# Performance work log

Measured on AMD Instinct MI355X. Metric: run time of the kernel, lower is better.

Reference implementation:

```python
import jax, jax.numpy as jnp
import numpy as np

DIM = 1024
HEADS = 16
HD = DIM // HEADS          # 64
HID = 4 * DIM              # 4096
TPF = 1374                 # tokens_per_frame
LR = 0.1
NS_ITERS = 5
TTT_STEPS = 2
B, S = 2, 4
SN = S * TPF               # 5496


def _newton_schulz(G, iters=NS_ITERS):
    """Muon Newton-Schulz orthogonalization (quintic iteration)."""
    a, b, c = 3.4445, -4.7750, 2.0315
    X = G / (jnp.linalg.norm(G) + 1e-7)
    transposed = G.shape[0] > G.shape[1]
    if transposed:
        X = X.T
    for _ in range(iters):
        A = X @ X.T                      # [m,m], m = min(rows, cols)
        X = a * X + (b * A + c * (A @ A)) @ X
    return X.T if transposed else X


def _muon_update(p, g):
    return p - LR * _newton_schulz(g)


def setup_inputs() -> dict:
    key = jax.random.key(0)
    ks = jax.random.split(key, 8)
    inp = {
        "x": jax.random.normal(ks[0], (B, SN, DIM), jnp.float32),
        "qkv_w": jax.random.normal(ks[1], (DIM, 3 * DIM), jnp.float32) * (DIM ** -0.5),
        "qkv_b": jnp.zeros((3 * DIM,), jnp.float32),
        "qn_scale": jnp.ones((HD,), jnp.float32),
        "qn_bias": jnp.zeros((HD,), jnp.float32),
        "kn_scale": jnp.ones((HD,), jnp.float32),
        "kn_bias": jnp.zeros((HD,), jnp.float32),
        # theta: lecun-normal scale (std = 1/sqrt(fan_in))
        "ttt_gate": jax.random.normal(ks[2], (DIM, HID), jnp.float32) * (DIM ** -0.5),
        "ttt_val": jax.random.normal(ks[3], (DIM, HID), jnp.float32) * (DIM ** -0.5),
        "ttt_proj": jax.random.normal(ks[4], (HID, DIM), jnp.float32) * (HID ** -0.5),
        "proj_w": jax.random.normal(ks[5], (DIM, DIM), jnp.float32) * (DIM ** -0.5),
        "proj_b": jnp.zeros((DIM,), jnp.float32),
    }
    return inp


def reference(x, qkv_w, qkv_b, qn_scale, qn_bias, kn_scale, kn_bias,
              ttt_gate, ttt_val, ttt_proj, proj_w, proj_b):
    Bx, SNx, _ = x.shape
    qkv = x @ qkv_w + qkv_b                       # [B, SN, 3*DIM]
    q, k, v = jnp.split(qkv, 3, axis=-1)
    q = q.reshape(Bx, SNx, HEADS, HD)
    k = k.reshape(Bx, SNx, HEADS, HD)
    # per-head L2 normalize then affine NormLayer (x*scale + bias)
    q = q / (jnp.linalg.norm(q, axis=-1, keepdims=True) + 1e-6) * qn_scale + qn_bias
    k = k / (jnp.linalg.norm(k, axis=-1, keepdims=True) + 1e-6) * kn_scale + kn_bias
    q_ttt = q.reshape(-1, DIM)                    # [B*SN, DIM]
    k_ttt = k.reshape(-1, DIM)
    # no short_conv param at init -> v_mixed is identity, so v_target == v
    v_ttt = v.reshape(-1, DIM)

    theta = {"gate": ttt_gate, "val": ttt_val, "proj": ttt_proj}

    def loss_fn(p):
        h = jax.nn.swish(k_ttt @ p["gate"]) * (k_ttt @ p["val"])   # [B*SN, HID]
        pred = h @ p["proj"]                                        # [B*SN, DIM]
        return jnp.mean((pred - v_ttt) ** 2)

    for _ in range(TTT_STEPS):
        grads = jax.grad(loss_fn)(theta)
        theta = {kk: _muon_update(theta[kk], grads[kk]) for kk in theta}

    h_q = jax.nn.swish(q_ttt @ theta["gate"]) * (q_ttt @ theta["val"])
    o = (h_q @ theta["proj"]) @ proj_w + proj_b
    return o.reshape(Bx, SNx, DIM)
```

## Files before the change

kernel.cpp:

```cpp
#include <hip/hip_runtime.h>
#include <stdint.h>

#define NTOK 10992
#define NTOKA 11264
#define FCHK 5632
#define PMi 4194304

typedef unsigned short u16;
typedef __attribute__((ext_vector_type(8))) __bf16 b8;
typedef __attribute__((ext_vector_type(4))) float f32x4;

__device__ __forceinline__ u16 f2b(float f) {
  union { float f; uint32_t u; } v; v.f = f;
  return (u16)((v.u + 0x7fffu + ((v.u >> 16) & 1u)) >> 16);
}
__device__ __forceinline__ float b2f(u16 b) {
  union { uint32_t u; float f; } v; v.u = ((uint32_t)b) << 16; return v.f;
}
__device__ __forceinline__ uint2 pk4(u16 a, u16 b, u16 c, u16 d) {
  uint2 r; r.x = (uint32_t)a | ((uint32_t)b << 16); r.y = (uint32_t)c | ((uint32_t)d << 16);
  return r;
}
__device__ __forceinline__ void gload16(const u16* g, u16* l) {
  __builtin_amdgcn_global_load_lds((const __attribute__((address_space(1))) void*)(const void*)g,
                                   (__attribute__((address_space(3))) void*)(void*)l, 16, 0, 0);
}

struct GA {
  const u16* A[3]; const u16* B[3];
  void* C[3]; u16* O1[3]; u16* OT[3];
  const void* E0[3]; const u16* E1[3];
  int lda[3], ldb[3];
  int M, N, K, ldc, ldo1, ldt, lde0, lde1;
  float p0, p1;
};

template <int EPI, int SPLIT>
__global__ __launch_bounds__(256, 2) void gemm_bt(GA g) {
  __shared__ u16 As[128 * 32];
  __shared__ u16 Bs[128 * 32];
  int bz = blockIdx.z, koff = 0, klen = g.K;
  if constexpr (SPLIT) { koff = (bz & 1) * (g.K >> 1); bz >>= 1; klen = g.K >> 1; }
  const u16* __restrict__ A = g.A[bz] + koff;
  const u16* __restrict__ B = g.B[bz] + koff;
  const int lda = g.lda[bz], ldb = g.ldb[bz];
  const int m0 = blockIdx.y * 128, n0 = blockIdx.x * 128;
  const int tid = threadIdx.x, w = tid >> 6, lane = tid & 63;
  const int wr = (w >> 1) * 64, wc = (w & 1) * 64;
  const int ln = lane & 15, lq = lane >> 4;

  f32x4 acc[4][4];
#pragma unroll
  for (int i = 0; i < 4; ++i)
#pragma unroll
    for (int j = 0; j < 4; ++j)
#pragma unroll
      for (int r = 0; r < 4; ++r) acc[i][j][r] = 0.f;

  const u16* Ag = A + (size_t)(m0 + 32 * w + (lane >> 2)) * lda + (lane & 3) * 8;
  const u16* Bg = B + (size_t)(n0 + 32 * w + (lane >> 2)) * ldb + (lane & 3) * 8;
  u16* AsW = &As[w * 1024];
  u16* BsW = &Bs[w * 1024];
  const int nkt = klen >> 5;

  for (int kt = 0; kt < nkt; ++kt) {
    __syncthreads();
    gload16(Ag, AsW);
    gload16(Ag + (size_t)16 * lda, AsW + 512);
    gload16(Bg, BsW);
    gload16(Bg + (size_t)16 * ldb, BsW + 512);
    Ag += 32; Bg += 32;
    __syncthreads();
    b8 af[4], bfr[4];
#pragma unroll
    for (int i = 0; i < 4; ++i) af[i] = *(const b8*)&As[(wr + i * 16 + ln) * 32 + lq * 8];
#pragma unroll
    for (int j = 0; j < 4; ++j) bfr[j] = *(const b8*)&Bs[(wc + j * 16 + ln) * 32 + lq * 8];
#pragma unroll
    for (int i = 0; i < 4; ++i)
#pragma unroll
      for (int j = 0; j < 4; ++j)
        acc[i][j] = __builtin_amdgcn_mfma_f32_16x16x32_bf16(af[i], bfr[j], acc[i][j], 0, 0, 0);
  }

  float* Cf = (float*)g.C[bz];
  u16* Cb = (u16*)g.C[bz];
  u16* O1 = g.O1[bz];
  u16* OT = g.OT[bz];
  const float* E0f = (const float*)g.E0[bz];
  const u16* E0b = (const u16*)g.E0[bz];
  const u16* E1b = g.E1[bz];

#pragma unroll
  for (int i = 0; i < 4; ++i) {
    const int mb = m0 + wr + i * 16 + lq * 4;
    if (mb >= g.M) continue;
#pragma unroll
    for (int j = 0; j < 4; ++j) {
      const int n = n0 + wc + j * 16 + ln;
      if (n >= g.N) continue;
      float vv[4];
#pragma unroll
      for (int r = 0; r < 4; ++r) vv[r] = acc[i][j][r];
      if constexpr (EPI == 0) {
#pragma unroll
        for (int r = 0; r < 4; ++r) Cb[(size_t)(mb + r) * g.ldc + n] = f2b(vv[r]);
      } else if constexpr (EPI == 1) {
        const float bias = E0f[n];
#pragma unroll
        for (int r = 0; r < 4; ++r) Cb[(size_t)(mb + r) * g.ldc + n] = f2b(vv[r] + bias);
      } else if constexpr (EPI == 5) {
        u16 cq[4], oq[4];
#pragma unroll
        for (int r = 0; r < 4; ++r) {
          const int m = mb + r;
          const float zg = b2f(E0b[(size_t)m * g.lde0 + n]);
          const float zv = b2f(E1b[(size_t)m * g.lde1 + n]);
          const float s = 1.f / (1.f + __expf(-zg));
          cq[r] = f2b(vv[r] * zv * s * (1.f + zg * (1.f - s)));
          oq[r] = f2b(vv[r] * zg * s);
        }
        *(uint2*)&Cb[(size_t)n * g.ldt + mb] = pk4(cq[0], cq[1], cq[2], cq[3]);
        *(uint2*)&O1[(size_t)n * g.ldt + mb] = pk4(oq[0], oq[1], oq[2], oq[3]);
      } else if constexpr (EPI == 8) {
#pragma unroll
        for (int r = 0; r < 4; ++r) atomicAdd(&Cf[(size_t)(mb + r) * g.ldc + n], vv[r]);
      } else if constexpr (EPI == 9) {
        u16 cq[4];
#pragma unroll
        for (int r = 0; r < 4; ++r) {
          const int m = mb + r;
          const u16 ub = f2b(g.p0 * b2f(E0b[(size_t)m * g.lde0 + n]) + vv[r]);
          Cb[(size_t)m * g.ldc + n] = ub;
          cq[r] = ub;
        }
        if (OT) *(uint2*)&OT[(size_t)n * g.ldt + mb] = pk4(cq[0], cq[1], cq[2], cq[3]);
      }
    }
  }
}

template <int EPI>
__global__ __launch_bounds__(256, 2) void gemm_gv(GA g) {
  __shared__ u16 As[128 * 32];
  __shared__ u16 Gs[128 * 32];
  __shared__ u16 Vs[128 * 32];
  const u16* __restrict__ A = g.A[0];
  const u16* __restrict__ G = g.B[0];
  const u16* __restrict__ V = g.B[1];
  const int lda = g.lda[0], ldb = g.ldb[0];
  const int m0 = blockIdx.y * 128, n0 = blockIdx.x * 128;
  const int tid = threadIdx.x, w = tid >> 6, lane = tid & 63;
  const int wr = (w >> 1) * 64, wc = (w & 1) * 64;
  const int ln = lane & 15, lq = lane >> 4;

  f32x4 ag[4][4], av[4][4];
#pragma unroll
  for (int i = 0; i < 4; ++i)
#pragma unroll
    for (int j = 0; j < 4; ++j)
#pragma unroll
      for (int r = 0; r < 4; ++r) { ag[i][j][r] = 0.f; av[i][j][r] = 0.f; }

  const u16* Agp = A + (size_t)(m0 + 32 * w + (lane >> 2)) * lda + (lane & 3) * 8;
  const u16* Ggp = G + (size_t)(n0 + 32 * w + (lane >> 2)) * ldb + (lane & 3) * 8;
  const u16* Vgp = V + (size_t)(n0 + 32 * w + (lane >> 2)) * ldb + (lane & 3) * 8;
  u16* AsW = &As[w * 1024];
  u16* GsW = &Gs[w * 1024];
  u16* VsW = &Vs[w * 1024];
  const int nkt = g.K >> 5;

  for (int kt = 0; kt < nkt; ++kt) {
    __syncthreads();
    gload16(Agp, AsW);
    gload16(Agp + (size_t)16 * lda, AsW + 512);
    gload16(Ggp, GsW);
    gload16(Ggp + (size_t)16 * ldb, GsW + 512);
    gload16(Vgp, VsW);
    gload16(Vgp + (size_t)16 * ldb, VsW + 512);
    Agp += 32; Ggp += 32; Vgp += 32;
    __syncthreads();
    b8 af[4], gf[4], vf[4];
#pragma unroll
    for (int i = 0; i < 4; ++i) af[i] = *(const b8*)&As[(wr + i * 16 + ln) * 32 + lq * 8];
#pragma unroll
    for (int j = 0; j < 4; ++j) gf[j] = *(const b8*)&Gs[(wc + j * 16 + ln) * 32 + lq * 8];
#pragma unroll
    for (int j = 0; j < 4; ++j) vf[j] = *(const b8*)&Vs[(wc + j * 16 + ln) * 32 + lq * 8];
#pragma unroll
    for (int i = 0; i < 4; ++i)
#pragma unroll
      for (int j = 0; j < 4; ++j) {
        ag[i][j] = __builtin_amdgcn_mfma_f32_16x16x32_bf16(af[i], gf[j], ag[i][j], 0, 0, 0);
        av[i][j] = __builtin_amdgcn_mfma_f32_16x16x32_bf16(af[i], vf[j], av[i][j], 0, 0, 0);
      }
  }

  u16* Zg = (u16*)g.C[0];
  u16* Zv = g.O1[0];
  u16* Hh = g.O1[1];
  u16* HT = g.OT[0];

#pragma unroll
  for (int i = 0; i < 4; ++i) {
    const int mb = m0 + wr + i * 16 + lq * 4;
    if (mb >= g.M) continue;
#pragma unroll
    for (int j = 0; j < 4; ++j) {
      const int n = n0 + wc + j * 16 + ln;
      if (n >= g.N) continue;
      u16 hq[4];
#pragma unroll
      for (int r = 0; r < 4; ++r) {
        const int m = mb + r;
        const float zg = ag[i][j][r];
        const float zv = av[i][j][r];
        const float s = 1.f / (1.f + __expf(-zg));
        const u16 hb = f2b(zg * s * zv);
        if constexpr (EPI == 0) {
// ... 68 lines not shown
    u16* Zv = ggv.O1[0];
    u16* Hh = ggv.O1[1];
    u16* HT = ggv.OT[0];
#pragma unroll
    for (int i = 0; i < 4; ++i) {
      const int mb = m0 + wr + i * 16 + lq * 4;
      if (mb >= ggv.M) continue;
#pragma unroll
      for (int j = 0; j < 4; ++j) {
        const int n = n0 + wc + j * 16 + ln;
        if (n >= ggv.N) continue;
        u16 hq[4];
#pragma unroll
        for (int r = 0; r < 4; ++r) {
          const int m = mb + r;
          const float zg = ag[i][j][r];
          const float zv = av[i][j][r];
          const float s = 1.f / (1.f + __expf(-zg));
          const u16 hb = f2b(zg * s * zv);
          Zg[(size_t)m * ggv.ldc + n] = f2b(zg);
          Zv[(size_t)m * ggv.ldc + n] = f2b(zv);
          Hh[(size_t)m * ggv.ldc + n] = hb;
          hq[r] = hb;
        }
        *(uint2*)&HT[(size_t)n * ggv.ldt + mb] = pk4(hq[0], hq[1], hq[2], hq[3]);
      }
    }
  } else {
    const int yy = (int)blockIdx.y - ysplit;
    int bz = yy >> 3;
    const int m0 = (yy & 7) * 128, n0 = blockIdx.x * 128;
    const int koff = (bz & 1) * (ggr.K >> 1); bz >>= 1;
    const int klen = ggr.K >> 1;
    const u16* __restrict__ A = ggr.A[bz] + koff;
    const u16* __restrict__ B = ggr.B[bz] + koff;
    const int lda = ggr.lda[bz], ldb = ggr.ldb[bz];
    f32x4 acc[4][4];
#pragma unroll
    for (int i = 0; i < 4; ++i)
#pragma unroll
      for (int j = 0; j < 4; ++j)
#pragma unroll
        for (int r = 0; r < 4; ++r) acc[i][j][r] = 0.f;
    const u16* Ag = A + (size_t)(m0 + 32 * w + (lane >> 2)) * lda + (lane & 3) * 8;
    const u16* Bg = B + (size_t)(n0 + 32 * w + (lane >> 2)) * ldb + (lane & 3) * 8;
    u16* AsW = &As[w * 1024];
    u16* BsW = &Bs[w * 1024];
    const int nkt = klen >> 5;
    for (int kt = 0; kt < nkt; ++kt) {
      __syncthreads();
      gload16(Ag, AsW);
      gload16(Ag + (size_t)16 * lda, AsW + 512);
      gload16(Bg, BsW);
      gload16(Bg + (size_t)16 * ldb, BsW + 512);
      Ag += 32; Bg += 32;
      __syncthreads();
      b8 af[4], bfr[4];
#pragma unroll
      for (int i = 0; i < 4; ++i) af[i] = *(const b8*)&As[(wr + i * 16 + ln) * 32 + lq * 8];
#pragma unroll
      for (int j = 0; j < 4; ++j) bfr[j] = *(const b8*)&Bs[(wc + j * 16 + ln) * 32 + lq * 8];
#pragma unroll
      for (int i = 0; i < 4; ++i)
#pragma unroll
        for (int j = 0; j < 4; ++j)
          acc[i][j] = __builtin_amdgcn_mfma_f32_16x16x32_bf16(af[i], bfr[j], acc[i][j], 0, 0, 0);
    }
    float* Cf = (float*)ggr.C[bz];
#pragma unroll
    for (int i = 0; i < 4; ++i) {
      const int mb = m0 + wr + i * 16 + lq * 4;
      if (mb >= ggr.M) continue;
#pragma unroll
      for (int j = 0; j < 4; ++j) {
        const int n = n0 + wc + j * 16 + ln;
        if (n >= ggr.N) continue;
#pragma unroll
        for (int r = 0; r < 4; ++r) atomicAdd(&Cf[(size_t)(mb + r) * ggr.ldc + n], acc[i][j][r]);
      }
    }
  }
}

template <int EPI>
__global__ __launch_bounds__(256, 2) void gemm64(GA g) {
  if constexpr (EPI == 10 || EPI == 11 || EPI == 12) {
    if (blockIdx.x > blockIdx.y) return;
  }
  __shared__ u16 As[64 * 32];
  __shared__ u16 Bs[64 * 32];
  const int bz = blockIdx.z;
  const u16* __restrict__ A = g.A[bz];
  const u16* __restrict__ B = g.B[bz];
  const int lda = g.lda[bz], ldb = g.ldb[bz];
  const int m0 = blockIdx.y * 64, n0 = blockIdx.x * 64;
  const int tid = threadIdx.x, w = tid >> 6, lane = tid & 63;
  const int wr = (w >> 1) * 32, wc = (w & 1) * 32;
  const int ln = lane & 15, lq = lane >> 4;

  f32x4 acc[2][2];
#pragma unroll
  for (int i = 0; i < 2; ++i)
#pragma unroll
    for (int j = 0; j < 2; ++j)
#pragma unroll
      for (int r = 0; r < 4; ++r) acc[i][j][r] = 0.f;

  const u16* Ag = A + (size_t)(m0 + 16 * w + (lane >> 2)) * lda + (lane & 3) * 8;
  const u16* Bg = B + (size_t)(n0 + 16 * w + (lane >> 2)) * ldb + (lane & 3) * 8;
  u16* AsW = &As[w * 512];
  u16* BsW = &Bs[w * 512];
  const int nkt = g.K >> 5;

  for (int kt = 0; kt < nkt; ++kt) {
    __syncthreads();
    gload16(Ag, AsW);
    gload16(Bg, BsW);
    Ag += 32; Bg += 32;
    __syncthreads();
    b8 af[2], bfr[2];
#pragma unroll
    for (int i = 0; i < 2; ++i) af[i] = *(const b8*)&As[(wr + i * 16 + ln) * 32 + lq * 8];
#pragma unroll
    for (int j = 0; j < 2; ++j) bfr[j] = *(const b8*)&Bs[(wc + j * 16 + ln) * 32 + lq * 8];
#pragma unroll
    for (int i = 0; i < 2; ++i)
#pragma unroll
      for (int j = 0; j < 2; ++j)
        acc[i][j] = __builtin_amdgcn_mfma_f32_16x16x32_bf16(af[i], bfr[j], acc[i][j], 0, 0, 0);
  }

  float* Cf = (float*)g.C[bz];
  u16* Cb = (u16*)g.C[bz];
  u16* OT = g.OT[bz];
  const float* E0f = (const float*)g.E0[bz];
  const u16* E0b = (const u16*)g.E0[bz];
  const u16* E1b = g.E1[bz];
  const bool offdiag = (blockIdx.x != blockIdx.y);

#pragma unroll
  for (int i = 0; i < 2; ++i) {
    const int mb = m0 + wr + i * 16 + lq * 4;
    if (mb >= g.M) continue;
#pragma unroll
    for (int j = 0; j < 2; ++j) {
      const int n = n0 + wc + j * 16 + ln;
      if (n >= g.N) continue;
      float vv[4];
#pragma unroll
      for (int r = 0; r < 4; ++r) vv[r] = acc[i][j][r];
      if constexpr (EPI == 0) {
#pragma unroll
        for (int r = 0; r < 4; ++r) Cb[(size_t)(mb + r) * g.ldc + n] = f2b(vv[r]);
      } else if constexpr (EPI == 2) {
        u16 cq[4];
#pragma unroll
        for (int r = 0; r < 4; ++r) {
          const int m = mb + r;
          const u16 ub = f2b((vv[r] - b2f(E0b[(size_t)m * g.lde0 + n])) * g.p0);
          Cb[(size_t)m * g.ldc + n] = ub;
          cq[r] = ub;
        }
        *(uint2*)&OT[(size_t)n * g.ldt + mb] = pk4(cq[0], cq[1], cq[2], cq[3]);
      } else if constexpr (EPI == 6) {
        const float bias = E0f[n];
#pragma unroll
        for (int r = 0; r < 4; ++r) Cf[(size_t)(mb + r) * g.ldc + n] = vv[r] + bias;
      } else if constexpr (EPI == 10) {
        u16 cq[4];
#pragma unroll
        for (int r = 0; r < 4; ++r) {
          cq[r] = f2b(vv[r]);
          Cb[(size_t)(mb + r) * g.ldc + n] = cq[r];
        }
        if (offdiag)
          *(uint2*)&Cb[(size_t)n * g.ldc + mb] = pk4(cq[0], cq[1], cq[2], cq[3]);
      } else if constexpr (EPI == 11) {
        u16 cq[4];
#pragma unroll
        for (int r = 0; r < 4; ++r) {
          cq[r] = f2b(g.p0 * b2f(E0b[(size_t)(mb + r) * g.lde0 + n]) + g.p1 * vv[r]);
          Cb[(size_t)(mb + r) * g.ldc + n] = cq[r];
        }
        if (offdiag)
          *(uint2*)&Cb[(size_t)n * g.ldc + mb] = pk4(cq[0], cq[1], cq[2], cq[3]);
      } else if constexpr (EPI == 12) {
        const uint2 t2u = *(const uint2*)&E1b[(size_t)n * g.lde1 + mb];
        const float t2v[4] = { b2f((u16)(t2u.x & 0xffff)), b2f((u16)(t2u.x >> 16)),
                               b2f((u16)(t2u.y & 0xffff)), b2f((u16)(t2u.y >> 16)) };
        u16 cq[4];
#pragma unroll
        for (int r = 0; r < 4; ++r) {
          const int m = mb + r;
          const float t1 = b2f(E1b[(size_t)m * g.lde1 + n]);
          const float a0 = b2f(E0b[(size_t)m * g.lde0 + n]);
          cq[r] = f2b(g.p0 * a0 + g.p1 * (t1 + t2v[r]) + vv[r]);
          Cb[(size_t)m * g.ldc + n] = cq[r];
        }
        if (offdiag)
          *(uint2*)&Cb[(size_t)n * g.ldc + mb] = pk4(cq[0], cq[1], cq[2], cq[3]);
      }
    }
  }
}

__global__ __launch_bounds__(256) void norm_qkv(const u16* __restrict__ qkvB,
    const float* __restrict__ qs, const float* __restrict__ qbi,
    const float* __restrict__ ks, const float* __restrict__ kbi,
    u16* __restrict__ qb, u16* __restrict__ kb, u16* __restrict__ vb) {
  const int tok = blockIdx.x;
  const int t = threadIdx.x;
  const int d = t * 4;
  const u16* row = qkvB + (size_t)tok * 3072;
  const uint2 qu = *(const uint2*)(row + d);
  const uint2 ku = *(const uint2*)(row + 1024 + d);
  *(uint2*)(vb + (size_t)tok * 1024 + d) = *(const uint2*)(row + 2048 + d);
  float q0 = b2f(qu.x & 0xffff), q1 = b2f(qu.x >> 16), q2 = b2f(qu.y & 0xffff), q3 = b2f(qu.y >> 16);
  float k0 = b2f(ku.x & 0xffff), k1 = b2f(ku.x >> 16), k2 = b2f(ku.y & 0xffff), k3 = b2f(ku.y >> 16);
  float sq = q0 * q0 + q1 * q1 + q2 * q2 + q3 * q3;
  float sk = k0 * k0 + k1 * k1 + k2 * k2 + k3 * k3;
  for (int off = 1; off < 16; off <<= 1) { sq += __shfl_xor(sq, off); sk += __shfl_xor(sk, off); }
  const float rq = 1.f / (sqrtf(sq) + 1e-6f);
  const float rk = 1.f / (sqrtf(sk) + 1e-6f);
  const int hd = d & 63;
  const float4 qsv = *(const float4*)(qs + hd);
  const float4 qbv = *(const float4*)(qbi + hd);
  const float4 ksv = *(const float4*)(ks + hd);
  const float4 kbv = *(const float4*)(kbi + hd);
  uint64_t pq = (uint64_t)f2b(q0 * rq * qsv.x + qbv.x)
              | ((uint64_t)f2b(q1 * rq * qsv.y + qbv.y) << 16)
              | ((uint64_t)f2b(q2 * rq * qsv.z + qbv.z) << 32)
              | ((uint64_t)f2b(q3 * rq * qsv.w + qbv.w) << 48);
  uint64_t pk = (uint64_t)f2b(k0 * rk * ksv.x + kbv.x)
              | ((uint64_t)f2b(k1 * rk * ksv.y + kbv.y) << 16)
              | ((uint64_t)f2b(k2 * rk * ksv.z + kbv.z) << 32)
              | ((uint64_t)f2b(k3 * rk * ksv.w + kbv.w) << 48);
  *(uint64_t*)(qb + (size_t)tok * 1024 + d) = pq;
  *(uint64_t*)(kb + (size_t)tok * 1024 + d) = pk;
}

__global__ __launch_bounds__(256) void tr_b16(const u16* __restrict__ in, u16* __restrict__ out,
                                              int Cin, int Rtot, int Rval,
                                              size_t inStr, size_t outStr) {
  const int b = blockIdx.z;
  in += (size_t)b * inStr; out += (size_t)b * outStr;
  __shared__ u16 t[32][33];
  const int c0 = blockIdx.x * 32, r0 = blockIdx.y * 32;
  const int tx = threadIdx.x, ty = threadIdx.y;
#pragma unroll
  for (int yy = 0; yy < 4; ++yy) {
    const int rr = ty * 4 + yy;
    const int r = r0 + rr;
    t[rr][tx] = (r < Rval) ? in[(size_t)r * Cin + c0 + tx] : (u16)0;
  }
  __syncthreads();
#pragma unroll
  for (int yy = 0; yy < 4; ++yy) {
    const int cc = ty * 4 + yy;
    out[(size_t)(c0 + cc) * Rtot + r0 + tx] = t[tx][cc];
  }
}

__global__ __launch_bounds__(256) void tr_f32b(const float* __restrict__ in, u16* __restrict__ out,
                                               int Cin, int Rtot) {
  __shared__ u16 t[32][33];
  const int c0 = blockIdx.x * 32, r0 = blockIdx.y * 32;
  const int tx = threadIdx.x, ty = threadIdx.y;
#pragma unroll
  for (int yy = 0; yy < 4; ++yy) {
    const int rr = ty * 4 + yy;
    t[rr][tx] = f2b(in[(size_t)(r0 + rr) * Cin + c0 + tx]);
  }
  __syncthreads();
#pragma unroll
  for (int yy = 0; yy < 4; ++yy) {
    const int cc = ty * 4 + yy;
    out[(size_t)(c0 + cc) * Rtot + r0 + tx] = t[tx][cc];
  }
}

__global__ void cvt_k(const float* __restrict__ in, u16* __restrict__ out, int n) {
  const int i = blockIdx.x * 256 + threadIdx.x;
  if (i < n) out[i] = f2b(in[i]);
}

__global__ void diag_k(float* __restrict__ out, int n, float val) {
  const int i = blockIdx.x * 256 + threadIdx.x;
  if (i < n) out[i] = val;
}

__global__ __launch_bounds__(256) void sumsq_k(const float* __restrict__ g, float* __restrict__ out) {
  const int b = blockIdx.y;
  const float* p = g + (size_t)b * PMi;
  float s = 0.f;
  for (int i = blockIdx.x * 256 + threadIdx.x; i < PMi; i += gridDim.x * 256) {
    float v = p[i]; s += v * v;
  }
  for (int off = 32; off > 0; off >>= 1) s += __shfl_xor(s, off);
  __shared__ float red[4];
  if ((threadIdx.x & 63) == 0) red[threadIdx.x >> 6] = s;
  __syncthreads();
  if (threadIdx.x == 0) atomicAdd(out + b, red[0] + red[1] + red[2] + red[3]);
}

__global__ __launch_bounds__(256) void scale_k(const float* __restrict__ g, const float* __restrict__ ss,
                                               u16* __restrict__ Xb) {
  const int b = blockIdx.y;
  const float r = 1.f / (sqrtf(ss[b]) + 1e-7f);
  const size_t o = (size_t)b * PMi;
  for (int i = blockIdx.x * 256 + threadIdx.x; i < PMi; i += gridDim.x * 256)
    Xb[o + i] = f2b(g[o + i] * r);
}

__global__ __launch_bounds__(256) void muon_apply(const u16* __restrict__ Xb_,
    u16* __restrict__ Gt, u16* __restrict__ Vt, u16* __restrict__ Pt, u16* __restrict__ Pb) {
  const int b = blockIdx.z;
  __shared__ float xs[32][33];
  __shared__ u16 ns[32][33];
  const int j0 = blockIdx.x * 32;
  const int i0 = blockIdx.y * 32;
  const u16* X = Xb_ + (size_t)b * PMi;
  const int tx = threadIdx.x, ty = threadIdx.y;
#pragma unroll
  for (int yy = 0; yy < 4; ++yy) {
    const int r = ty * 4 + yy;
    xs[r][tx] = b2f(X[(size_t)(i0 + r) * 4096 + j0 + tx]);
  }
  __syncthreads();
  if (b < 2) {
    u16* T = b ? Vt : Gt;
#pragma unroll
    for (int yy = 0; yy < 4; ++yy) {
      const int rr = ty * 4 + yy;
      const size_t idx = (size_t)(j0 + rr) * 1024 + i0 + tx;
      T[idx] = f2b(b2f(T[idx]) - 0.1f * xs[tx][rr]);
    }
  } else {
#pragma unroll
    for (int yy = 0; yy < 4; ++yy) {
      const int rr = ty * 4 + yy;
      const size_t idx = (size_t)(j0 + rr) * 1024 + i0 + tx;
      const float nv = b2f(Pb[idx]) - 0.1f * xs[tx][rr];
      const u16 nb = f2b(nv);
      Pb[idx] = nb;
      ns[rr][tx] = nb;
    }
    __syncthreads();
#pragma unroll
    for (int yy = 0; yy < 4; ++yy) {
      const int rr = ty * 4 + yy;
      Pt[(size_t)(i0 + rr) * 4096 + j0 + tx] = ns[tx][rr];
    }
  }
}

static GA mk(const u16* A, const u16* B, void* C, int M, int N, int K,
             int lda, int ldb, int ldc) {
  GA a{};
  a.A[0] = a.A[1] = a.A[2] = A;
  a.B[0] = a.B[1] = a.B[2] = B;
  a.C[0] = a.C[1] = a.C[2] = C;
  a.lda[0] = a.lda[1] = a.lda[2] = lda;
  a.ldb[0] = a.ldb[1] = a.ldb[2] = ldb;
  a.M = M; a.N = N; a.K = K; a.ldc = ldc;
  return a;
}

extern "C" void kernel_launch(void* const* d_in, const int* in_sizes, int n_in,
                              void* d_out, int out_size, void* d_ws, size_t ws_size,
                              hipStream_t stream) {
  (void)in_sizes; (void)n_in;
  const float* x      = (const float*)d_in[0];
  const float* qkv_w  = (const float*)d_in[1];
  const float* qkv_b  = (const float*)d_in[2];
  const float* qn_s   = (const float*)d_in[3];
  const float* qn_b   = (const float*)d_in[4];
  const float* kn_s   = (const float*)d_in[5];
  const float* kn_b   = (const float*)d_in[6];
  const float* g_gate = (const float*)d_in[7];
  const float* g_val  = (const float*)d_in[8];
  const float* g_proj = (const float*)d_in[9];
  const float* proj_w = (const float*)d_in[10];
  const float* proj_b = (const float*)d_in[11];
  float* out = (float*)d_out;

  const size_t PM = PMi;
  const size_t TD = (size_t)NTOKA * 1024;

  const size_t NEED1 = 253231360 + 4096;
  const size_t NEED2 = 127926528 + 177209344 + 4096;
  const size_t NEEDP = 351273216 + 8192;
  if (ws_size < NEED1) {
    diag_k<<<dim3((out_size + 255) / 256), dim3(256), 0, stream>>>(out, out_size,
                                                                   (float)(ws_size >> 20));
    return;
  }
  const int CHKr = (ws_size >= NEED2) ? 2816 : 1408;
  const int PAIRED = (ws_size >= NEEDP) ? 1 : 0;

  char* p = (char*)d_ws;
  auto carve = [&](size_t bytes) { char* r = p; p += (bytes + 255) & ~(size_t)255; return (void*)r; };
  auto cdiv = [](int a, int b) { return (a + b - 1) / b; };

  u16* Gt     = (u16*)carve(PM * 2);
  u16* Vt     = (u16*)carve(PM * 2);
  u16* Pt     = (u16*)carve(PM * 2);
  u16* Pb     = (u16*)carve(PM * 2);
  u16* projWt = (u16*)carve(1048576ull * 2);
  u16* qb     = (u16*)carve(TD * 2);
  u16* kb     = (u16*)carve(TD * 2);
  u16* vT     = (u16*)carve(TD * 2);
  u16* kT     = (u16*)carve(TD * 2);
  float* ssq  = (float*)carve(256);
  char* arena = p;

  u16* xb     = (u16*)arena;
  u16* qkvWt  = (u16*)(arena + 23068672);
  u16* qkvB   = (u16*)(arena + 29360128);
  u16* vb_tmp = (u16*)(arena + 96894976);
  const size_t CB = (size_t)CHKr * 4096 * 2;
  const size_t DP = (size_t)CHKr * 1024 * 2;
  u16* zg     = (u16*)arena;
  u16* zv     = (u16*)(arena + CB);
  u16* hh0    = (u16*)(arena + 2 * CB);
  u16* hT0    = (u16*)(arena + 3 * CB);
  u16* dzvT   = (u16*)(arena + 4 * CB);
  u16* dpredT = (u16*)(arena + 5 * CB);
  u16* dpredb = (u16*)(arena + 5 * CB + DP);
  float* gAll = (float*)(arena + 5 * CB + 2 * DP);
  u16* hh1    = PAIRED ? (u16*)(arena + 5 * CB + 2 * DP + 3 * PM * 4) : hh0;
  u16* hT1    = PAIRED ? (u16*)(arena + 6 * CB + 2 * DP + 3 * PM * 4) : hT0;
  u16* hhA[2] = {hh0, hh1};
  u16* hTA[2] = {hT0, hT1};
  u16* XAb  = (u16*)arena;
  u16* XAbT = (u16*)(arena + 25165824);
  u16* XBb  = (u16*)(arena + 50331648);
  u16* XBbT = (u16*)(arena + 75497472);
  u16* Ab   = (u16*)(arena + 100663296);
  u16* Wb   = (u16*)(arena + 106954752);
  u16* Tb   = (u16*)(arena + 113246208);
  const int FCN  = (CHKr >= 2816) ? 1 : 2;
  const int FBLK = (FCN == 1) ? NTOK : FCHK;
  u16* hbuf = (u16*)arena;
  u16* oc   = (u16*)(arena + ((FCN == 1) ? 92274688ull : 46137344ull));

  const dim3 blk(256), tb32(32, 8);
  const float inv2 = 2.0f / (10992.0f * 1024.0f);
  const float nsa = 3.4445f, nsb = -4.7750f, nsc = 2.0315f;

  cvt_k<<<dim3(43968), blk, 0, stream>>>(x, xb, NTOK * 1024);
  cvt_k<<<dim3(16384), blk, 0, stream>>>(g_proj, Pb, (int)PM);
  tr_f32b<<<dim3(96, 32), tb32, 0, stream>>>(qkv_w, qkvWt, 3072, 1024);
  tr_f32b<<<dim3(32, 32), tb32, 0, stream>>>(proj_w, projWt, 1024, 1024);
  tr_f32b<<<dim3(128, 32), tb32, 0, stream>>>(g_gate, Gt, 4096, 1024);
  tr_f32b<<<dim3(128, 32), tb32, 0, stream>>>(g_val, Vt, 4096, 1024);
  tr_f32b<<<dim3(32, 128), tb32, 0, stream>>>(g_proj, Pt, 1024, 4096);

  {
    GA a = mk(xb, qkvWt, qkvB, NTOK, 3072, 1024, 1024, 1024, 3072);
    a.E0[0] = a.E0[1] = a.E0[2] = qkv_b;
    gemm_bt<1, 0><<<dim3(24, 86, 1), blk, 0, stream>>>(a);
  }
  norm_qkv<<<dim3(NTOK), blk, 0, stream>>>(qkvB, qn_s, qn_b, kn_s, kn_b, qb, kb, vb_tmp);
  tr_b16<<<dim3(32, 352, 1), tb32, 0, stream>>>(kb, kT, 1024, NTOKA, NTOK, 0, 0);
  tr_b16<<<dim3(32, 352, 1), tb32, 0, stream>>>(vb_tmp, vT, 1024, NTOKA, NTOK, 0, 0);

  for (int step = 0; step < 2; ++step) {
    hipMemsetAsync(gAll, 0, 3 * PM * 4, stream);
    int havePend = 0;
    GA pendGA{};
    for (int ci = 0, c0 = 0; c0 < NTOK; ++ci, c0 += CHKr) {
      const int vc = (NTOK - c0 < CHKr) ? (NTOK - c0) : CHKr;
      const int mt = cdiv(vc, 128);
      const u16* kc = kb + (size_t)c0 * 1024;
      u16* hhp = hhA[ci & 1];
      u16* hTp = hTA[ci & 1];
      if (vc < CHKr)
        hipMemsetAsync(hTp, 0, CB, stream);
      {
        GA agv{};
        agv.A[0] = kc; agv.lda[0] = 1024;
        agv.B[0] = Gt; agv.B[1] = Vt; agv.ldb[0] = 1024;
        agv.C[0] = zg; agv.O1[0] = zv; agv.O1[1] = hhp; agv.OT[0] = hTp;
        agv.M = vc; agv.N = 4096; agv.K = 1024; agv.ldc = 4096; agv.ldt = CHKr;
        if (PAIRED && havePend) {
          fused_gg<<<dim3(32, mt + 48, 1), blk, 0, stream>>>(pendGA, agv, mt);
          havePend = 0;
        } else {
          gemm_gv<0><<<dim3(32, mt, 1), blk, 0, stream>>>(agv);
        }
      }
      if (vc < CHKr) {
        hipMemsetAsync(dzvT, 0, CB, stream);
        hipMemsetAsync(dpredT, 0, DP, stream);
      }
      {
        GA a = mk(Pt, hhp, dpredT, 1024, vc, 4096, 4096, 4096, CHKr);
        a.OT[0] = dpredb; a.ldt = 1024;
        a.E0[0] = vT + c0; a.lde0 = NTOKA; a.p0 = inv2;
        gemm64<2><<<dim3(cdiv(vc, 64), 16, 1), blk, 0, stream>>>(a);
      }
      if (vc < CHKr)
        hipMemsetAsync(hhp, 0, CB, stream);
      {
        GA a = mk(dpredb, Pb, hhp, vc, 4096, 1024, 1024, 1024, 0);
        a.O1[0] = dzvT; a.ldt = CHKr;
        a.E0[0] = zg; a.lde0 = 4096; a.E1[0] = zv; a.lde1 = 4096;
        gemm_bt<5, 0><<<dim3(32, mt, 1), blk, 0, stream>>>(a);
      }
      {
        GA a{};
        a.A[0] = kT + c0; a.A[1] = kT + c0; a.A[2] = dpredT;
        a.lda[0] = NTOKA; a.lda[1] = NTOKA; a.lda[2] = CHKr;
        a.B[0] = hhp; a.B[1] = dzvT; a.B[2] = hTp;
        a.ldb[0] = a.ldb[1] = a.ldb[2] = CHKr;
        a.C[0] = gAll; a.C[1] = gAll + PM; a.C[2] = gAll + 2 * PM;
        a.M = 1024; a.N = 4096; a.K = CHKr; a.ldc = 4096;
        const int last = (c0 + CHKr >= NTOK);
        if (PAIRED && !last) { pendGA = a; havePend = 1; }
        else gemm_bt<8, 1><<<dim3(32, 8, 6), blk, 0, stream>>>(a);
      }
    }
    hipMemsetAsync(ssq, 0, 16, stream);
    sumsq_k<<<dim3(512, 3), blk, 0, stream>>>(gAll, ssq);
    scale_k<<<dim3(2048, 3), blk, 0, stream>>>(gAll, ssq, XAb);
    tr_b16<<<dim3(128, 32, 3), tb32, 0, stream>>>(XAb, XAbT, 4096, 1024, 1024, PM, PM);

    u16* Xi_b = XAb; u16* Xi_bT = XAbT;
    u16* Xo_b = XBb; u16* Xo_bT = XBbT;
    {
      GA a{};
      for (int b = 0; b < 3; ++b) {
        a.A[b] = Xi_b + (size_t)b * PM; a.B[b] = Xi_b + (size_t)b * PM;
        a.C[b] = Ab + (size_t)b * 1048576;
        a.lda[b] = 4096; a.ldb[b] = 4096;
      }
      a.M = 1024; a.N = 1024; a.K = 4096; a.ldc = 1024;
      gemm64<10><<<dim3(16, 16, 3), blk, 0, stream>>>(a);
    }
    for (int it = 0; it < 5; ++it) {
      {
        GA a{};
        for (int b = 0; b < 3; ++b) {
          a.A[b] = Ab + (size_t)b * 1048576; a.B[b] = Ab + (size_t)b * 1048576;
          a.C[b] = Wb + (size_t)b * 1048576; a.E0[b] = Ab + (size_t)b * 1048576;
          a.lda[b] = 1024; a.ldb[b] = 1024;
        }
        a.M = 1024; a.N = 1024; a.K = 1024; a.ldc = 1024; a.lde0 = 1024;
        a.p0 = nsb; a.p1 = nsc;
        gemm64<11><<<dim3(16, 16, 3), blk, 0, stream>>>(a);
      }
      {
        GA a{};
        for (int b = 0; b < 3; ++b) {
          a.A[b] = Wb + (size_t)b * 1048576; a.B[b] = Xi_bT + (size_t)b * PM;
          a.C[b] = Xo_b + (size_t)b * PM;
          a.OT[b] = (it == 4) ? nullptr : (Xo_bT + (size_t)b * PM);
          a.E0[b] = Xi_b + (size_t)b * PM;
          a.lda[b] = 1024; a.ldb[b] = 1024;
        }
        a.M = 1024; a.N = 4096; a.K = 1024; a.ldc = 4096; a.ldt = 1024;
        a.lde0 = 4096; a.p0 = nsa;
        gemm_bt<9, 0><<<dim3(32, 8, 3), blk, 0, stream>>>(a);
      }
      if (it < 4) {
        {
          GA a{};
          for (int b = 0; b < 3; ++b) {
            a.A[b] = Wb + (size_t)b * 1048576; a.B[b] = Ab + (size_t)b * 1048576;
            a.C[b] = Tb + (size_t)b * 1048576;
            a.lda[b] = 1024; a.ldb[b] = 1024;
          }
          a.M = 1024; a.N = 1024; a.K = 1024; a.ldc = 1024;
          gemm64<0><<<dim3(16, 16, 3), blk, 0, stream>>>(a);
        }
        {
          GA a{};
          for (int b = 0; b < 3; ++b) {
            a.A[b] = Tb + (size_t)b * 1048576; a.B[b] = Wb + (size_t)b * 1048576;
            a.C[b] = Ab + (size_t)b * 1048576;
            a.E0[b] = Ab + (size_t)b * 1048576; a.E1[b] = Tb + (size_t)b * 1048576;
            a.lda[b] = 1024; a.ldb[b] = 1024;
          }
          a.M = 1024; a.N = 1024; a.K = 1024; a.ldc = 1024;
          a.lde0 = 1024; a.lde1 = 1024;
          a.p0 = nsa * nsa; a.p1 = nsa;
          gemm64<12><<<dim3(16, 16, 3), blk, 0, stream>>>(a);
        }
      }
      u16* tb = Xi_b; Xi_b = Xo_b; Xo_b = tb;
      u16* tt = Xi_bT; Xi_bT = Xo_bT; Xo_bT = tt;
    }
    muon_apply<<<dim3(128, 32, 3), tb32, 0, stream>>>(Xi_b, Gt, Vt, Pt, Pb);
  }

  for (int fc = 0; fc < FCN; ++fc) {
    const int c0 = fc * FBLK;
    const int vc = (NTOK - c0 < FBLK) ? (NTOK - c0) : FBLK;
    const int mt = cdiv(vc, 128), mt64 = cdiv(vc, 64);
    const u16* qc = qb + (size_t)c0 * 1024;
    {
      GA a{};
      a.A[0] = qc; a.lda[0] = 1024;
      a.B[0] = Gt; a.B[1] = Vt; a.ldb[0] = 1024;
      a.C[0] = hbuf;
      a.M = vc; a.N = 4096; a.K = 1024; a.ldc = 4096;
      gemm_gv<1><<<dim3(32, mt, 1), blk, 0, stream>>>(a);
    }
    gemm64<0><<<dim3(16, mt64, 1), blk, 0, stream>>>(
        mk(hbuf, Pt, oc, vc, 1024, 4096, 4096, 4096, 1024));
    {
      GA a = mk(oc, projWt, out + (size_t)c0 * 1024, vc, 1024, 1024, 1024, 1024, 1024);
      a.E0[0] = proj_b;
      gemm64<6><<<dim3(16, mt64, 1), blk, 0, stream>>>(a);
    }
  }
}
```

Measured before the change: 6.079 ms.

## Accumulate Newton-Schulz as polynomial in small matrix; fold proj_w into TTT proj

Rewrites the Newton-Schulz loop so the 1024x4096 iterate is never updated per iteration. Instead, a 1024x1024 multiplier matrix is accumulated (starting from a*I plus W) and applied to the initial X with one wide GEMM at the end, which also performs the muon update in its epilogue. It also fuses scaling with transposition, runs the independent T and M small GEMMs in one launch, and precomputes proj_w times the updated ttt_proj so the final output needs one fewer large token GEMM. This trades repeated 4096-wide GEMMs for 1024-sized ones, with extra bf16 rounding in the accumulated multiplier and a reworked workspace plan.

```diff
diff --git a/kernel.cpp b/kernel.cpp
--- a/kernel.cpp
+++ b/kernel.cpp
@@ -3,7 +3,6 @@
 
 #define NTOK 10992
 #define NTOKA 11264
-#define FCHK 5632
 #define PMi 4194304
 
 typedef unsigned short u16;
@@ -86,7 +85,6 @@
   float* Cf = (float*)g.C[bz];
   u16* Cb = (u16*)g.C[bz];
   u16* O1 = g.O1[bz];
-  u16* OT = g.OT[bz];
   const float* E0f = (const float*)g.E0[bz];
   const u16* E0b = (const u16*)g.E0[bz];
   const u16* E1b = g.E1[bz];
@@ -122,19 +120,25 @@
         }
         *(uint2*)&Cb[(size_t)n * g.ldt + mb] = pk4(cq[0], cq[1], cq[2], cq[3]);
         *(uint2*)&O1[(size_t)n * g.ldt + mb] = pk4(oq[0], oq[1], oq[2], oq[3]);
+      } else if constexpr (EPI == 6) {
+        const float bias = E0f[n];
+#pragma unroll
+        for (int r = 0; r < 4; ++r) Cf[(size_t)(mb + r) * g.ldc + n] = vv[r] + bias;
       } else if constexpr (EPI == 8) {
 #pragma unroll
         for (int r = 0; r < 4; ++r) atomicAdd(&Cf[(size_t)(mb + r) * g.ldc + n], vv[r]);
-      } else if constexpr (EPI == 9) {
-        u16 cq[4];
-#pragma unroll
-        for (int r = 0; r < 4; ++r) {
-          const int m = mb + r;
-          const u16 ub = f2b(g.p0 * b2f(E0b[(size_t)m * g.lde0 + n]) + vv[r]);
-          Cb[(size_t)m * g.ldc + n] = ub;
-          cq[r] = ub;
-        }
-        if (OT) *(uint2*)&OT[(size_t)n * g.ldt + mb] = pk4(cq[0], cq[1], cq[2], cq[3]);
+      } else if constexpr (EPI == 16) {
+        uint2 old = *(const uint2*)&Cb[(size_t)n * 1024 + mb];
+        u16 nq[4];
+        nq[0] = f2b(b2f((u16)(old.x & 0xffff)) - 0.1f * vv[0]);
+        nq[1] = f2b(b2f((u16)(old.x >> 16)) - 0.1f * vv[1]);
+        nq[2] = f2b(b2f((u16)(old.y & 0xffff)) - 0.1f * vv[2]);
+        nq[3] = f2b(b2f((u16)(old.y >> 16)) - 0.1f * vv[3]);
+        *(uint2*)&Cb[(size_t)n * 1024 + mb] = pk4(nq[0], nq[1], nq[2], nq[3]);
+        if (O1) {
+#pragma unroll
+          for (int r = 0; r < 4; ++r) O1[(size_t)(mb + r) * 4096 + n] = nq[r];
+        }
       }
     }
   }
@@ -369,6 +373,74 @@
   }
 }
 
+__global__ __launch_bounds__(256, 2) void fused_mt(GA gt, GA gm) {
+  __shared__ u16 As[64 * 32];
+  __shared__ u16 Bs[64 * 32];
+  const int bz = blockIdx.z;
+  const int mp = ((int)blockIdx.y >= 16) ? 1 : 0;
+  const GA& g = mp ? gm : gt;
+  const int m0 = ((int)blockIdx.y - (mp ? 16 : 0)) * 64, n0 = blockIdx.x * 64;
+  const u16* __restrict__ A = g.A[bz];
+  const u16* __restrict__ B = g.B[bz];
+  const int lda = g.lda[bz], ldb = g.ldb[bz];
+  const int tid = threadIdx.x, w = tid >> 6, lane = tid & 63;
+  const int wr = (w >> 1) * 32, wc = (w & 1) * 32;
+  const int ln = lane & 15, lq = lane >> 4;
+
+  f32x4 acc[2][2];
+#pragma unroll
+  for (int i = 0; i < 2; ++i)
+#pragma unroll
+    for (int j = 0; j < 2; ++j)
+#pragma unroll
+      for (int r = 0; r < 4; ++r) acc[i][j][r] = 0.f;
+
+  const u16* Ag = A + (size_t)(m0 + 16 * w + (lane >> 2)) * lda + (lane & 3) * 8;
+  const u16* Bg = B + (size_t)(n0 + 16 * w + (lane >> 2)) * ldb + (lane & 3) * 8;
+  u16* AsW = &As[w * 512];
+  u16* BsW = &Bs[w * 512];
+  const int nkt = g.K >> 5;
+
+  for (int kt = 0; kt < nkt; ++kt) {
+    __syncthreads();
+    gload16(Ag, AsW);
+    gload16(Bg, BsW);
+    Ag += 32; Bg += 32;
+    __syncthreads();
+    b8 af[2], bfr[2];
+#pragma unroll
+    for (int i = 0; i < 2; ++i) af[i] = *(const b8*)&As[(wr + i * 16 + ln) * 32 + lq * 8];
+#pragma unroll
+    for (int j = 0; j < 2; ++j) bfr[j] = *(const b8*)&Bs[(wc + j * 16 + ln) * 32 + lq * 8];
+#pragma unroll
+    for (int i = 0; i < 2; ++i)
+#pragma unroll
+      for (int j = 0; j < 2; ++j)
+        acc[i][j] = __builtin_amdgcn_mfma_f32_16x16x32_bf16(af[i], bfr[j], acc[i][j], 0, 0, 0);
+  }
+
+  u16* Cb = (u16*)g.C[bz];
+  const u16* E0b = (const u16*)g.E0[bz];
+#pragma unroll
+  for (int i = 0; i < 2; ++i) {
+    const int mb = m0 + wr + i * 16 + lq * 4;
+#pragma unroll
+    for (int j = 0; j < 2; ++j) {
+      const int n = n0 + wc + j * 16 + ln;
+      if (mp) {
+#pragma unroll
+        for (int r = 0; r < 4; ++r) {
+          const int m = mb + r;
+          Cb[(size_t)m * g.ldc + n] = f2b(g.p0 * b2f(E0b[(size_t)m * g.lde0 + n]) + acc[i][j][r]);
+        }
+      } else {
+#pragma unroll
+        for (int r = 0; r < 4; ++r) Cb[(size_t)(mb + r) * g.ldc + n] = f2b(acc[i][j][r]);
+      }
+    }
+  }
+}
+
 template <int EPI>
 __global__ __launch_bounds__(256, 2) void gemm64(GA g) {
   if constexpr (EPI == 10 || EPI == 11 || EPI == 12) {
@@ -417,10 +489,8 @@
         acc[i][j] = __builtin_amdgcn_mfma_f32_16x16x32_bf16(af[i], bfr[j], acc[i][j], 0, 0, 0);
   }
 
-  float* Cf = (float*)g.C[bz];
   u16* Cb = (u16*)g.C[bz];
   u16* OT = g.OT[bz];
-  const float* E0f = (const float*)g.E0[bz];
   const u16* E0b = (const u16*)g.E0[bz];
   const u16* E1b = g.E1[bz];
   const bool offdiag = (blockIdx.x != blockIdx.y);
@@ -449,10 +519,6 @@
           cq[r] = ub;
         }
         *(uint2*)&OT[(size_t)n * g.ldt + mb] = pk4(cq[0], cq[1], cq[2], cq[3]);
-      } else if constexpr (EPI == 6) {
-        const float bias = E0f[n];
-#pragma unroll
-        for (int r = 0; r < 4; ++r) Cf[(size_t)(mb + r) * g.ldc + n] = vv[r] + bias;
       } else if constexpr (EPI == 10) {
         u16 cq[4];
 #pragma unroll
@@ -486,6 +552,13 @@
         }
         if (offdiag)
           *(uint2*)&Cb[(size_t)n * g.ldc + mb] = pk4(cq[0], cq[1], cq[2], cq[3]);
+      } else if constexpr (EPI == 15) {
+        const uint2 eu = *(const uint2*)&E0b[(size_t)n * g.lde0 + mb];
+        const float e4[4] = { b2f((u16)(eu.x & 0xffff)), b2f((u16)(eu.x >> 16)),
+                              b2f((u16)(eu.y & 0xffff)), b2f((u16)(eu.y >> 16)) };
+#pragma unroll
+        for (int r = 0; r < 4; ++r)
+          Cb[(size_t)(mb + r) * g.ldc + n] = f2b(g.p0 * e4[r] + vv[r]);
       }
     }
   }
@@ -576,6 +649,14 @@
   if (i < n) out[i] = val;
 }
 
+__global__ void addI_k(const u16* __restrict__ W, u16* __restrict__ M, float a) {
+  const int i = blockIdx.x * 256 + threadIdx.x;
+  const size_t o = (size_t)blockIdx.y * 1048576;
+  u16 v = W[o + i];
+  if ((i >> 10) == (i & 1023)) v = f2b(a + b2f(v));
+  M[o + i] = v;
+}
+
 __global__ __launch_bounds__(256) void sumsq_k(const float* __restrict__ g, float* __restrict__ out) {
   const int b = blockIdx.y;
   const float* p = g + (size_t)b * PMi;
@@ -590,54 +671,28 @@
   if (threadIdx.x == 0) atomicAdd(out + b, red[0] + red[1] + red[2] + red[3]);
 }
 
-__global__ __launch_bounds__(256) void scale_k(const float* __restrict__ g, const float* __restrict__ ss,
-                                               u16* __restrict__ Xb) {
-  const int b = blockIdx.y;
+__global__ __launch_bounds__(256) void scale_tr(const float* __restrict__ g, const float* __restrict__ ss,
+                                                u16* __restrict__ Xb, u16* __restrict__ XbT) {
+  const int b = blockIdx.z;
+  __shared__ u16 t[32][33];
   const float r = 1.f / (sqrtf(ss[b]) + 1e-7f);
-  const size_t o = (size_t)b * PMi;
-  for (int i = blockIdx.x * 256 + threadIdx.x; i < PMi; i += gridDim.x * 256)
-    Xb[o + i] = f2b(g[o + i] * r);
-}
-
-__global__ __launch_bounds__(256) void muon_apply(const u16* __restrict__ Xb_,
-    u16* __restrict__ Gt, u16* __restrict__ Vt, u16* __restrict__ Pt, u16* __restrict__ Pb) {
-  const int b = blockIdx.z;
-  __shared__ float xs[32][33];
-  __shared__ u16 ns[32][33];
-  const int j0 = blockIdx.x * 32;
-  const int i0 = blockIdx.y * 32;
-  const u16* X = Xb_ + (size_t)b * PMi;
+  const float* G = g + (size_t)b * PMi;
+  u16* X = Xb + (size_t)b * PMi;
+  u16* XT = XbT + (size_t)b * PMi;
+  const int j0 = blockIdx.x * 32, i0 = blockIdx.y * 32;
   const int tx = threadIdx.x, ty = threadIdx.y;
 #pragma unroll
   for (int yy = 0; yy < 4; ++yy) {
-    const int r = ty * 4 + yy;
-    xs[r][tx] = b2f(X[(size_t)(i0 + r) * 4096 + j0 + tx]);
+    const int rr = ty * 4 + yy;
+    const u16 v = f2b(G[(size_t)(i0 + rr) * 4096 + j0 + tx] * r);
+    X[(size_t)(i0 + rr) * 4096 + j0 + tx] = v;
+    t[rr][tx] = v;
   }
   __syncthreads();
-  if (b < 2) {
-    u16* T = b ? Vt : Gt;
-#pragma unroll
-    for (int yy = 0; yy < 4; ++yy) {
-      const int rr = ty * 4 + yy;
-      const size_t idx = (size_t)(j0 + rr) * 1024 + i0 + tx;
-      T[idx] = f2b(b2f(T[idx]) - 0.1f * xs[tx][rr]);
-    }
-  } else {
-#pragma unroll
-    for (int yy = 0; yy < 4; ++yy) {
-      const int rr = ty * 4 + yy;
-      const size_t idx = (size_t)(j0 + rr) * 1024 + i0 + tx;
-      const float nv = b2f(Pb[idx]) - 0.1f * xs[tx][rr];
-      const u16 nb = f2b(nv);
-      Pb[idx] = nb;
-      ns[rr][tx] = nb;
-    }
-    __syncthreads();
-#pragma unroll
-    for (int yy = 0; yy < 4; ++yy) {
-      const int rr = ty * 4 + yy;
-      Pt[(size_t)(i0 + rr) * 4096 + j0 + tx] = ns[tx][rr];
-    }
+#pragma unroll
+  for (int yy = 0; yy < 4; ++yy) {
+    const int cc = ty * 4 + yy;
+    XT[(size_t)(j0 + cc) * 1024 + i0 + tx] = t[tx][cc];
   }
 }
 
@@ -673,17 +728,27 @@
 
   const size_t PM = PMi;
   const size_t TD = (size_t)NTOKA * 1024;
-
-  const size_t NEED1 = 253231360 + 4096;
-  const size_t NEED2 = 127926528 + 177209344 + 4096;
-  const size_t NEEDP = 351273216 + 8192;
-  if (ws_size < NEED1) {
+  const size_t PERS = 127926528ull;
+
+  auto needP = [&](int chk) {
+    return PERS + 7ull * (size_t)chk * 8192 + 2ull * (size_t)chk * 2048 + 50331648ull + 8192;
+  };
+  auto needU = [&](int chk) {
+    return PERS + 5ull * (size_t)chk * 8192 + 2ull * (size_t)chk * 2048 + 50331648ull + 4096;
+  };
+  int CHKr, PAIRED;
+  if      (ws_size >= needP(5632)) { CHKr = 5632; PAIRED = 1; }
+  else if (ws_size >= needU(5632)) { CHKr = 5632; PAIRED = 0; }
+  else if (ws_size >= needP(2816)) { CHKr = 2816; PAIRED = 1; }
+  else if (ws_size >= needP(2560)) { CHKr = 2560; PAIRED = 1; }
+  else if (ws_size >= needP(2304)) { CHKr = 2304; PAIRED = 1; }
+  else if (ws_size >= needP(2048)) { CHKr = 2048; PAIRED = 1; }
+  else if (ws_size >= needU(1408)) { CHKr = 1408; PAIRED = 0; }
+  else {
     diag_k<<<dim3((out_size + 255) / 256), dim3(256), 0, stream>>>(out, out_size,
                                                                    (float)(ws_size >> 20));
     return;
   }
-  const int CHKr = (ws_size >= NEED2) ? 2816 : 1408;
-  const int PAIRED = (ws_size >= NEEDP) ? 1 : 0;
 
   char* p = (char*)d_ws;
   auto carve = [&](size_t bytes) { char* r = p; p += (bytes + 255) & ~(size_t)255; return (void*)r; };
@@ -721,15 +786,13 @@
   u16* hTA[2] = {hT0, hT1};
   u16* XAb  = (u16*)arena;
   u16* XAbT = (u16*)(arena + 25165824);
-  u16* XBb  = (u16*)(arena + 50331648);
-  u16* XBbT = (u16*)(arena + 75497472);
-  u16* Ab   = (u16*)(arena + 100663296);
-  u16* Wb   = (u16*)(arena + 106954752);
-  u16* Tb   = (u16*)(arena + 113246208);
-  const int FCN  = (CHKr >= 2816) ? 1 : 2;
-  const int FBLK = (FCN == 1) ? NTOK : FCHK;
+  u16* Ab   = (u16*)(arena + 50331648);
+  u16* Wb   = (u16*)(arena + 56623104);
+  u16* Tb   = (u16*)(arena + 62914560);
+  u16* Mb0  = (u16*)(arena + 69206016);
+  u16* Mb1  = (u16*)(arena + 75497472);
   u16* hbuf = (u16*)arena;
-  u16* oc   = (u16*)(arena + ((FCN == 1) ? 92274688ull : 46137344ull));
+  u16* PWt  = (u16*)(arena + 92274688);
 
   const dim3 blk(256), tb32(32, 8);
   const float inv2 = 2.0f / (10992.0f * 1024.0f);
@@ -810,15 +873,12 @@
     }
     hipMemsetAsync(ssq, 0, 16, stream);
     sumsq_k<<<dim3(512, 3), blk, 0, stream>>>(gAll, ssq);
-    scale_k<<<dim3(2048, 3), blk, 0, stream>>>(gAll, ssq, XAb);
-    tr_b16<<<dim3(128, 32, 3), tb32, 0, stream>>>(XAb, XAbT, 4096, 1024, 1024, PM, PM);
-
-    u16* Xi_b = XAb; u16* Xi_bT = XAbT;
-    u16* Xo_b = XBb; u16* Xo_bT = XBbT;
+    scale_tr<<<dim3(128, 32, 3), tb32, 0, stream>>>(gAll, ssq, XAb, XAbT);
+
     {
       GA a{};
       for (int b = 0; b < 3; ++b) {
-        a.A[b] = Xi_b + (size_t)b * PM; a.B[b] = Xi_b + (size_t)b * PM;
+        a.A[b] = XAb + (size_t)b * PM; a.B[b] = XAb + (size_t)b * PM;
         a.C[b] = Ab + (size_t)b * 1048576;
         a.lda[b] = 4096; a.ldb[b] = 4096;
       }
@@ -837,20 +897,8 @@
         a.p0 = nsb; a.p1 = nsc;
         gemm64<11><<<dim3(16, 16, 3), blk, 0, stream>>>(a);
       }
-      {
-        GA a{};
-        for (int b = 0; b < 3; ++b) {
-          a.A[b] = Wb + (size_t)b * 1048576; a.B[b] = Xi_bT + (size_t)b * PM;
-          a.C[b] = Xo_b + (size_t)b * PM;
-          a.OT[b] = (it == 4) ? nullptr : (Xo_bT + (size_t)b * PM);
-          a.E0[b] = Xi_b + (size_t)b * PM;
-          a.lda[b] = 1024; a.ldb[b] = 1024;
-        }
-        a.M = 1024; a.N = 4096; a.K = 1024; a.ldc = 4096; a.ldt = 1024;
-        a.lde0 = 4096; a.p0 = nsa;
-        gemm_bt<9, 0><<<dim3(32, 8, 3), blk, 0, stream>>>(a);
-      }
-      if (it < 4) {
+      if (it == 0) {
+        addI_k<<<dim3(4096, 3), blk, 0, stream>>>(Wb, Mb0, nsa);
         {
           GA a{};
           for (int b = 0; b < 3; ++b) {
@@ -861,45 +909,71 @@
           a.M = 1024; a.N = 1024; a.K = 1024; a.ldc = 1024;
           gemm64<0><<<dim3(16, 16, 3), blk, 0, stream>>>(a);
         }
-        {
-          GA a{};
-          for (int b = 0; b < 3; ++b) {
-            a.A[b] = Tb + (size_t)b * 1048576; a.B[b] = Wb + (size_t)b * 1048576;
-            a.C[b] = Ab + (size_t)b * 1048576;
-            a.E0[b] = Ab + (size_t)b * 1048576; a.E1[b] = Tb + (size_t)b * 1048576;
-            a.lda[b] = 1024; a.ldb[b] = 1024;
-          }
-          a.M = 1024; a.N = 1024; a.K = 1024; a.ldc = 1024;
-          a.lde0 = 1024; a.lde1 = 1024;
-          a.p0 = nsa * nsa; a.p1 = nsa;
-          gemm64<12><<<dim3(16, 16, 3), blk, 0, stream>>>(a);
-        }
-      }
-      u16* tb = Xi_b; Xi_b = Xo_b; Xo_b = tb;
-      u16* tt = Xi_bT; Xi_bT = Xo_bT; Xo_bT = tt;
-    }
-    muon_apply<<<dim3(128, 32, 3), tb32, 0, stream>>>(Xi_b, Gt, Vt, Pt, Pb);
-  }
-
-  for (int fc = 0; fc < FCN; ++fc) {
-    const int c0 = fc * FBLK;
-    const int vc = (NTOK - c0 < FBLK) ? (NTOK - c0) : FBLK;
-    const int mt = cdiv(vc, 128), mt64 = cdiv(vc, 64);
-    const u16* qc = qb + (size_t)c0 * 1024;
+      } else if (it < 4) {
+        u16* Mti = (it & 1) ? Mb0 : Mb1;
+        u16* Mto = (it & 1) ? Mb1 : Mb0;
+        GA gt{}, gm{};
+        for (int b = 0; b < 3; ++b) {
+          gt.A[b] = Wb + (size_t)b * 1048576; gt.B[b] = Ab + (size_t)b * 1048576;
+          gt.C[b] = Tb + (size_t)b * 1048576;
+          gt.lda[b] = 1024; gt.ldb[b] = 1024;
+          gm.A[b] = Mti + (size_t)b * 1048576; gm.B[b] = Wb + (size_t)b * 1048576;
+          gm.C[b] = Mto + (size_t)b * 1048576; gm.E0[b] = Mti + (size_t)b * 1048576;
+          gm.lda[b] = 1024; gm.ldb[b] = 1024;
+        }
+        gt.M = gt.N = 1024; gt.K = 1024; gt.ldc = 1024;
+        gm.M = gm.N = 1024; gm.K = 1024; gm.ldc = 1024; gm.lde0 = 1024; gm.p0 = nsa;
+        fused_mt<<<dim3(16, 32, 3), blk, 0, stream>>>(gt, gm);
+      } else {
+        GA a{};
+        for (int b = 0; b < 3; ++b) {
+          a.A[b] = Wb + (size_t)b * 1048576; a.B[b] = Mb1 + (size_t)b * 1048576;
+          a.C[b] = Mb0 + (size_t)b * 1048576; a.E0[b] = Mb1 + (size_t)b * 1048576;
+          a.lda[b] = 1024; a.ldb[b] = 1024;
+        }
+        a.M = 1024; a.N = 1024; a.K = 1024; a.ldc = 1024; a.lde0 = 1024; a.p0 = nsa;
+        gemm64<15><<<dim3(16, 16, 3), blk, 0, stream>>>(a);
+      }
+      if (it < 4) {
+        GA a{};
+        for (int b = 0; b < 3; ++b) {
+          a.A[b] = Tb + (size_t)b * 1048576; a.B[b] = Wb + (size_t)b * 1048576;
+          a.C[b] = Ab + (size_t)b * 1048576;
+          a.E0[b] = Ab + (size_t)b * 1048576; a.E1[b] = Tb + (size_t)b * 1048576;
+          a.lda[b] = 1024; a.ldb[b] = 1024;
+        }
+        a.M = 1024; a.N = 1024; a.K = 1024; a.ldc = 1024;
+        a.lde0 = 1024; a.lde1 = 1024;
+        a.p0 = nsa * nsa; a.p1 = nsa;
+        gemm64<12><<<dim3(16, 16, 3), blk, 0, stream>>>(a);
+      }
+    }
     {
       GA a{};
-      a.A[0] = qc; a.lda[0] = 1024;
-      a.B[0] = Gt; a.B[1] = Vt; a.ldb[0] = 1024;
-      a.C[0] = hbuf;
-      a.M = vc; a.N = 4096; a.K = 1024; a.ldc = 4096;
-      gemm_gv<1><<<dim3(32, mt, 1), blk, 0, stream>>>(a);
-    }
-    gemm64<0><<<dim3(16, mt64, 1), blk, 0, stream>>>(
-        mk(hbuf, Pt, oc, vc, 1024, 4096, 4096, 4096, 1024));
-    {
-      GA a = mk(oc, projWt, out + (size_t)c0 * 1024, vc, 1024, 1024, 1024, 1024, 1024);
-      a.E0[0] = proj_b;
-      gemm64<6><<<dim3(16, mt64, 1), blk, 0, stream>>>(a);
-    }
-  }
-}
+      for (int b = 0; b < 3; ++b) {
+        a.A[b] = Mb0 + (size_t)b * 1048576; a.B[b] = XAbT + (size_t)b * PM;
+        a.lda[b] = 1024; a.ldb[b] = 1024;
+      }
+      a.C[0] = Gt; a.C[1] = Vt; a.C[2] = Pb;
+      a.O1[0] = nullptr; a.O1[1] = nullptr; a.O1[2] = Pt;
+      a.M = 1024; a.N = 4096; a.K = 1024; a.ldc = 1024;
+      gemm_bt<16, 0><<<dim3(32, 8, 3), blk, 0, stream>>>(a);
+    }
+  }
+
+  gemm_bt<0, 0><<<dim3(32, 8, 1), blk, 0, stream>>>(
+      mk(projWt, Pb, PWt, 1024, 4096, 1024, 1024, 1024, 4096));
+  {
+    GA a{};
+    a.A[0] = qb; a.lda[0] = 1024;
+    a.B[0] = Gt; a.B[1] = Vt; a.ldb[0] = 1024;
+    a.C[0] = hbuf;
+    a.M = NTOK; a.N = 4096; a.K = 1024; a.ldc = 4096;
+    gemm_gv<1><<<dim3(32, 86, 1), blk, 0, stream>>>(a);
+  }
+  {
+    GA a = mk(hbuf, PWt, out, NTOK, 1024, 4096, 4096, 4096, 1024);
+    a.E0[0] = proj_b;
+    gemm_bt<6, 0><<<dim3(8, 86, 1), blk, 0, stream>>>(a);
+  }
+}
```

New measurement: 5.622 ms. 1.08x faster.
